# Optimization experiments

Measured on AMD Instinct MI355X. Metric: run time of the kernel, lower is better.

The kernel has to match this reference:

```python
import jax, jax.numpy as jnp
import numpy as np

N_NODES = 100000
N_EDGES = 400000
D = 128           # vector_dim
N_GRAPHS = 4096
N_LAYERS = 5
IN_FEAT = 11


def setup_inputs() -> dict:
    key = jax.random.key(0)
    ks = jax.random.split(key, 6)
    x = jax.random.uniform(ks[0], (N_NODES, IN_FEAT), dtype=jnp.float32)
    edge_index = jax.random.randint(ks[1], (2, N_EDGES), 0, N_NODES, dtype=jnp.int64)
    batch = jnp.sort(jax.random.randint(ks[2], (N_NODES,), 0, N_GRAPHS, dtype=jnp.int64))
    # expansion Linear(11, D)
    We = jax.random.normal(ks[3], (IN_FEAT, D), dtype=jnp.float32) * (1.0 / np.sqrt(IN_FEAT))
    be = jnp.zeros((D,), dtype=jnp.float32)
    # stacked GCNConv weights/biases for 5 layers
    Wg = jax.random.normal(ks[4], (N_LAYERS, D, D), dtype=jnp.float32) * (1.0 / np.sqrt(D))
    bg = jnp.zeros((N_LAYERS, D), dtype=jnp.float32)
    return {"x": x, "edge_index": edge_index, "batch": batch, "num_graphs": N_GRAPHS,
            "We": We, "be": be, "Wg": Wg, "bg": bg}


def reference(x, edge_index, batch, num_graphs, We, be, Wg, bg):
    n = x.shape[0]
    src, dst = edge_index[0], edge_index[1]
    # GCNConv(improved=True): self-loop weight 2 -> deg[i] = in_degree + 2
    deg = jax.ops.segment_sum(jnp.ones((src.shape[0],), x.dtype), dst, num_segments=n) + 2.0
    dinv = deg ** -0.5
    enorm = dinv[src] * dinv[dst]          # per-edge symmetric norm [E]
    self_norm = 2.0 * dinv * dinv          # self-loop contribution [N]

    h = jnp.log(x + 1.0) @ We + be         # expansion [N, D]
    for l in range(Wg.shape[0]):
        t = h @ Wg[l]                      # [N, D]
        agg = jax.ops.segment_sum(t[src] * enorm[:, None], dst, num_segments=n)
        agg = agg + self_norm[:, None] * t + bg[l]
        h = h + jax.nn.relu(agg)           # residual; dropout = identity (eval)
    return jax.ops.segment_sum(h, batch, num_segments=num_graphs)  # global_add_pool [G, D]
```

## Files before the change

### kernel.cpp

```cpp
#include <hip/hip_runtime.h>
#include <hip/hip_bf16.h>

#define NN 100000
#define NE 400000
#define DD 128
#define NG 4096
#define NL 5
#define NF 11
#define GROWS 100096

typedef __attribute__((ext_vector_type(8))) __bf16 bf16x8;
typedef __attribute__((ext_vector_type(4))) float f32x4;


__global__ void deg_kernel(const int* __restrict__ ei, int* __restrict__ deg) {
    int e = blockIdx.x * 256 + threadIdx.x;
    if (e < NE) atomicAdd(&deg[ei[NE + e]], 1);
}

__global__ void scan1_kernel(const int* __restrict__ deg, int* __restrict__ off,
                             int* __restrict__ bsums) {
    __shared__ int lds[256];
    int tid = threadIdx.x, b = blockIdx.x;
    int base = b * 1024 + tid * 4;
    int v[4];
#pragma unroll
    for (int q = 0; q < 4; ++q) {
        int i = base + q;
        v[q] = (i < NN) ? deg[i] : 0;
    }
    int s = v[0] + v[1] + v[2] + v[3];
    lds[tid] = s;
    __syncthreads();
    for (int o = 1; o < 256; o <<= 1) {
        int t2 = (tid >= o) ? lds[tid - o] : 0;
        __syncthreads();
        lds[tid] += t2;
        __syncthreads();
    }
    int p = lds[tid] - s;
#pragma unroll
    for (int q = 0; q < 4; ++q) {
        int i = base + q;
        if (i < NN) off[i] = p;
        p += v[q];
    }
    if (tid == 255) bsums[b] = lds[255];
}

__global__ void scan2_kernel(int* __restrict__ bsums, int nb) {
    __shared__ int lds[128];
    int tid = threadIdx.x;
    int v = (tid < nb) ? bsums[tid] : 0;
    lds[tid] = v;
    __syncthreads();
    for (int o = 1; o < 128; o <<= 1) {
        int t2 = (tid >= o) ? lds[tid - o] : 0;
        __syncthreads();
        lds[tid] += t2;
        __syncthreads();
    }
    if (tid < nb) bsums[tid] = lds[tid] - v;
}

__global__ void finish_kernel(int* __restrict__ off, const int* __restrict__ bsums,
                              const int* __restrict__ deg, float* __restrict__ dinv) {
    int i = blockIdx.x * 256 + threadIdx.x;
    if (i == 0) off[NN] = NE;
    if (i < NN) {
        off[i] += bsums[i >> 10];
        dinv[i] = rsqrtf((float)deg[i] + 2.0f);
    }
}

__global__ void fill_kernel(const int* __restrict__ ei, const int* __restrict__ off,
                            int* __restrict__ cursor, int2* __restrict__ csr,
                            const float* __restrict__ dinv) {
    int e = blockIdx.x * 256 + threadIdx.x;
    if (e >= NE) return;
    int s = ei[e];
    int d = ei[NE + e];
    int pos = off[d] + atomicAdd(&cursor[d], 1);
    csr[pos] = make_int2(s, __float_as_int(dinv[s] * dinv[d]));
}


__global__ void wpack_kernel(const float* __restrict__ Wg, unsigned short* __restrict__ whi,
                             unsigned short* __restrict__ wlo) {
    int t = blockIdx.x * 256 + threadIdx.x;
    int l = t >> 14, r = t & 16383;
    int k = r >> 7, n = r & 127;
    float w = Wg[(size_t)l * 16384 + k * 128 + n];
    __bf16 hb = (__bf16)w;
    float lo = w - (float)hb;
    __bf16 lb = (__bf16)lo;
    int ft = n >> 4, kc = k >> 5, lane = (((k >> 3) & 3) << 4) | (n & 15), i = k & 7;
    size_t idx = (size_t)l * 16384 + (((ft * 4 + kc) * 64 + lane) * 8 + i);
    whi[idx] = __builtin_bit_cast(unsigned short, hb);
    wlo[idx] = __builtin_bit_cast(unsigned short, lb);
}


__global__ __launch_bounds__(256) void expand_kernel(const float* __restrict__ x,
                                                     const float* __restrict__ We,
                                                     const float* __restrict__ be,
                                                     float* __restrict__ h) {
    __shared__ float ls[2 * NF];
    const int tid = threadIdx.x;
    const int node0 = blockIdx.x * 2;
    if (tid < 2 * NF) ls[tid] = __logf(x[(size_t)node0 * NF + tid] + 1.0f);
    __syncthreads();
    const int row = tid >> 7, j = tid & 127;
    float acc = be[j];
#pragma unroll
    for (int f = 0; f < NF; ++f) {
        acc = fmaf(ls[row * NF + f], We[f * DD + j], acc);
    }
    h[(size_t)(node0 + row) * DD + j] = acc;
}


__global__ __launch_bounds__(256) void agg_kernel(const float* __restrict__ h,
                                                  unsigned short* __restrict__ gbh,
                                                  unsigned short* __restrict__ gbl,
                                                  const int* __restrict__ off,
                                                  const int2* __restrict__ csr,
                                                  const float* __restrict__ dinv) {
    const int tid = threadIdx.x;
    const int node = blockIdx.x * 8 + (tid >> 5);
    const int jj = tid & 31;
    const float4* __restrict__ h4 = (const float4*)h;

    float di = dinv[node];
    float sn = 2.0f * di * di;
    float4 hv = h4[(size_t)node * 32 + jj];
    float4 acc = make_float4(sn * hv.x, sn * hv.y, sn * hv.z, sn * hv.w);

    const int e0 = off[node];
    const int e1 = off[node + 1];
#pragma unroll 1
    for (int e = e0; e < e1; e += 4) {
        const int eL = e1 - 1;
        int2 r0 = csr[e];
        int2 r1 = csr[min(e + 1, eL)];
        int2 r2 = csr[min(e + 2, eL)];
        int2 r3 = csr[min(e + 3, eL)];
        float4 v0 = h4[(size_t)r0.x * 32 + jj];
        float4 v1 = h4[(size_t)r1.x * 32 + jj];
        float4 v2 = h4[(size_t)r2.x * 32 + jj];
        float4 v3 = h4[(size_t)r3.x * 32 + jj];
        float w0 = __int_as_float(r0.y);
        float w1 = (e + 1 < e1) ? __int_as_float(r1.y) : 0.f;
        float w2 = (e + 2 < e1) ? __int_as_float(r2.y) : 0.f;
        float w3 = (e + 3 < e1) ? __int_as_float(r3.y) : 0.f;
        acc.x = fmaf(w0, v0.x, acc.x); acc.y = fmaf(w0, v0.y, acc.y);
        acc.z = fmaf(w0, v0.z, acc.z); acc.w = fmaf(w0, v0.w, acc.w);
        acc.x = fmaf(w1, v1.x, acc.x); acc.y = fmaf(w1, v1.y, acc.y);
        acc.z = fmaf(w1, v1.z, acc.z); acc.w = fmaf(w1, v1.w, acc.w);
        acc.x = fmaf(w2, v2.x, acc.x); acc.y = fmaf(w2, v2.y, acc.y);
        acc.z = fmaf(w2, v2.z, acc.z); acc.w = fmaf(w2, v2.w, acc.w);
        acc.x = fmaf(w3, v3.x, acc.x); acc.y = fmaf(w3, v3.y, acc.y);
        acc.z = fmaf(w3, v3.z, acc.z); acc.w = fmaf(w3, v3.w, acc.w);
    }

    __bf16 h0 = (__bf16)acc.x; __bf16 l0 = (__bf16)(acc.x - (float)h0);
    __bf16 h1 = (__bf16)acc.y; __bf16 l1 = (__bf16)(acc.y - (float)h1);
    __bf16 h2 = (__bf16)acc.z; __bf16 l2 = (__bf16)(acc.z - (float)h2);
    __bf16 h3 = (__bf16)acc.w; __bf16 l3 = (__bf16)(acc.w - (float)h3);
    const int tile = node >> 4;
    const int kc = jj >> 3;
    const int kg = (jj >> 1) & 3;
    const int i0 = (jj & 1) * 4;
    const int lanep = (kg << 4) | (node & 15);
    size_t base = (((size_t)tile * 4 + kc) * 64 + lanep) * 8 + i0;
    ushort4 hs = make_ushort4(__builtin_bit_cast(unsigned short, h0),
                              __builtin_bit_cast(unsigned short, h1),
                              __builtin_bit_cast(unsigned short, h2),
                              __builtin_bit_cast(unsigned short, h3));
    ushort4 ls = make_ushort4(__builtin_bit_cast(unsigned short, l0),
                              __builtin_bit_cast(unsigned short, l1),
                              __builtin_bit_cast(unsigned short, l2),
                              __builtin_bit_cast(unsigned short, l3));
    *(ushort4*)(gbh + base) = hs;
    *(ushort4*)(gbl + base) = ls;
}


__global__ __launch_bounds__(256) void mfma_gemm(const unsigned short* __restrict__ gbh,
                                                 const unsigned short* __restrict__ gbl,
                                                 float* __restrict__ h,
                                                 const unsigned short* __restrict__ whi,
                                                 const unsigned short* __restrict__ wlo,
                                                 const float* __restrict__ b) {
    const int lane = threadIdx.x & 63;
    const int wv = threadIdx.x >> 6;
    const int nbase = blockIdx.x * 64 + wv * 16;
    const size_t tbase = ((size_t)(nbase >> 4) * 4 * 64 + lane) * 8;

    bf16x8 gh[4], gl[4];
#pragma unroll
    for (int kc = 0; kc < 4; ++kc) {
        gh[kc] = *(const bf16x8*)(gbh + tbase + kc * 512);
        gl[kc] = *(const bf16x8*)(gbl + tbase + kc * 512);
    }

    f32x4 c[8];
#pragma unroll
    for (int ft = 0; ft < 8; ++ft) c[ft] = (f32x4){0.f, 0.f, 0.f, 0.f};

#pragma unroll
    for (int kc = 0; kc < 4; ++kc) {
#pragma unroll
        for (int ft = 0; ft < 8; ++ft) {
            size_t boff = (size_t)(((ft * 4 + kc) * 64 + lane) * 8);
            bf16x8 wh = *(const bf16x8*)(whi + boff);
            bf16x8 wl = *(const bf16x8*)(wlo + boff);
            c[ft] = __builtin_amdgcn_mfma_f32_16x16x32_bf16(wh, gh[kc], c[ft], 0, 0, 0);
            c[ft] = __builtin_amdgcn_mfma_f32_16x16x32_bf16(wl, gh[kc], c[ft], 0, 0, 0);
            c[ft] = __builtin_amdgcn_mfma_f32_16x16x32_bf16(wh, gl[kc], c[ft], 0, 0, 0);
        }
    }

    const int node = nbase + (lane & 15);
    const int f0 = (lane >> 4) * 4;
    if (node < NN) {
#pragma unroll
        for (int ft = 0; ft < 8; ++ft) {
            size_t o = (size_t)node * DD + ft * 16 + f0;
            float4 hv = *(const float4*)(h + o);
            float4 bv = *(const float4*)(b + ft * 16 + f0);
            hv.x += fmaxf(c[ft][0] + bv.x, 0.f);
            hv.y += fmaxf(c[ft][1] + bv.y, 0.f);
            hv.z += fmaxf(c[ft][2] + bv.z, 0.f);
            hv.w += fmaxf(c[ft][3] + bv.w, 0.f);
            *(float4*)(h + o) = hv;
        }
    }
}


__global__ void pool_kernel(const float* __restrict__ h, const int* __restrict__ batch,
                            float* __restrict__ out) {
    int j = threadIdx.x;
    int n0 = blockIdx.x * 64;
    float acc = 0.f;
    int prev = -1;
    for (int n = 0; n < 64; ++n) {
        int i = n0 + n;
        if (i >= NN) break;
        int bi = batch[i];
        if (bi != prev) {
            if (prev >= 0) atomicAdd(&out[(size_t)prev * DD + j], acc);
            acc = 0.f;
            prev = bi;
        }
        acc += h[(size_t)i * DD + j];
    }
    if (prev >= 0) atomicAdd(&out[(size_t)prev * DD + j], acc);
}


static inline size_t align_up(size_t x, size_t a) { return (x + a - 1) & ~(a - 1); }

extern "C" void kernel_launch(void* const* d_in, const int* in_sizes, int n_in,
                              void* d_out, int out_size, void* d_ws, size_t ws_size,
                              hipStream_t stream) {
    const float* x   = (const float*)d_in[0];
    const int*   ei  = (const int*)d_in[1];
    const int*   bat = (const int*)d_in[2];
    const float* We  = (const float*)d_in[4];
    const float* be  = (const float*)d_in[5];
    const float* Wg  = (const float*)d_in[6];
    const float* bg  = (const float*)d_in[7];
    float* out = (float*)d_out;

    char* p = (char*)d_ws;
    size_t o = 0;
    float* h = (float*)(p + o);       o = align_up(o + (size_t)NN * DD * 4, 512);
    unsigned short* gbh = (unsigned short*)(p + o); o = align_up(o + (size_t)GROWS * DD * 2, 512);
    unsigned short* gbl = (unsigned short*)(p + o); o = align_up(o + (size_t)GROWS * DD * 2, 512);
    float* dinv = (float*)(p + o);    o = align_up(o + (size_t)NN * 4, 512);
    int* deg = (int*)(p + o);         o = align_up(o + (size_t)NN * 4, 512);
    int* cursor = (int*)(p + o);      o = align_up(o + (size_t)NN * 4, 512);
    int* off = (int*)(p + o);         o = align_up(o + (size_t)(NN + 1) * 4, 512);
    int* bsums = (int*)(p + o);       o = align_up(o + 512, 512);
    int2* csr = (int2*)(p + o);       o = align_up(o + (size_t)NE * 8, 512);
    unsigned short* whi = (unsigned short*)(p + o); o = align_up(o + (size_t)NL * 16384 * 2, 512);
    unsigned short* wlo = (unsigned short*)(p + o); o = align_up(o + (size_t)NL * 16384 * 2, 512);
    (void)ws_size; (void)in_sizes; (void)n_in; (void)out_size;

    const int GRID_E = (NE + 255) / 256;
    const int GRID_SCAN1 = (NN + 1023) / 1024;
    const int GRID_N256 = (NN + 255) / 256;
    const int GRID_EXP = NN / 2;
    const int GRID_AGG = NN / 8;
    const int GRID_GEMM = GROWS / 64;
    const int GRID_POOL = (NN + 63) / 64;
    const int GRID_WPACK = NL * 16384 / 256;

    hipMemsetAsync(deg, 0, (size_t)NN * 4, stream);
    hipMemsetAsync(cursor, 0, (size_t)NN * 4, stream);
    hipMemsetAsync(out, 0, (size_t)NG * DD * 4, stream);

    deg_kernel<<<GRID_E, 256, 0, stream>>>(ei, deg);
    scan1_kernel<<<GRID_SCAN1, 256, 0, stream>>>(deg, off, bsums);
    scan2_kernel<<<1, 128, 0, stream>>>(bsums, GRID_SCAN1);
    finish_kernel<<<GRID_N256, 256, 0, stream>>>(off, bsums, deg, dinv);
    fill_kernel<<<GRID_E, 256, 0, stream>>>(ei, off, cursor, csr, dinv);
    wpack_kernel<<<GRID_WPACK, 256, 0, stream>>>(Wg, whi, wlo);

    expand_kernel<<<GRID_EXP, 256, 0, stream>>>(x, We, be, h);

    for (int l = 0; l < NL; ++l) {
        agg_kernel<<<GRID_AGG, 256, 0, stream>>>(h, gbh, gbl, off, csr, dinv);
        mfma_gemm<<<GRID_GEMM, 256, 0, stream>>>(gbh, gbl, h,
                                                 whi + (size_t)l * 16384,
                                                 wlo + (size_t)l * 16384,
                                                 bg + (size_t)l * DD);
    }

    pool_kernel<<<GRID_POOL, 128, 0, stream>>>(h, bat, out);
}
```

Baseline: 601.9 us.

## Interleave two nodes per group in aggregation and drop CSR cursor array

The aggregation kernel now has each 32-lane group process two adjacent nodes, issuing eight independent gathers per iteration so more memory requests are in flight. The CSR fill uses atomicAdd directly on the offset array, which turns it into end offsets and removes the separate cursor buffer and its memset. Edges past a node's range are masked to zero weight, but the loop runs until both nodes finish, so some loads are wasted when the two degrees differ.

```diff
diff --git a/kernel.cpp b/kernel.cpp
--- a/kernel.cpp
+++ b/kernel.cpp
@@ -66,21 +66,19 @@
 __global__ void finish_kernel(int* __restrict__ off, const int* __restrict__ bsums,
                               const int* __restrict__ deg, float* __restrict__ dinv) {
     int i = blockIdx.x * 256 + threadIdx.x;
-    if (i == 0) off[NN] = NE;
     if (i < NN) {
         off[i] += bsums[i >> 10];
         dinv[i] = rsqrtf((float)deg[i] + 2.0f);
     }
 }
 
-__global__ void fill_kernel(const int* __restrict__ ei, const int* __restrict__ off,
-                            int* __restrict__ cursor, int2* __restrict__ csr,
-                            const float* __restrict__ dinv) {
+__global__ void fill_kernel(const int* __restrict__ ei, int* __restrict__ off,
+                            int2* __restrict__ csr, const float* __restrict__ dinv) {
     int e = blockIdx.x * 256 + threadIdx.x;
     if (e >= NE) return;
     int s = ei[e];
     int d = ei[NE + e];
-    int pos = off[d] + atomicAdd(&cursor[d], 1);
+    int pos = atomicAdd(&off[d], 1);
     csr[pos] = make_int2(s, __float_as_int(dinv[s] * dinv[d]));
 }
 
@@ -120,49 +118,9 @@
 }
 
 
-__global__ __launch_bounds__(256) void agg_kernel(const float* __restrict__ h,
-                                                  unsigned short* __restrict__ gbh,
-                                                  unsigned short* __restrict__ gbl,
-                                                  const int* __restrict__ off,
-                                                  const int2* __restrict__ csr,
-                                                  const float* __restrict__ dinv) {
-    const int tid = threadIdx.x;
-    const int node = blockIdx.x * 8 + (tid >> 5);
-    const int jj = tid & 31;
-    const float4* __restrict__ h4 = (const float4*)h;
-
-    float di = dinv[node];
-    float sn = 2.0f * di * di;
-    float4 hv = h4[(size_t)node * 32 + jj];
-    float4 acc = make_float4(sn * hv.x, sn * hv.y, sn * hv.z, sn * hv.w);
-
-    const int e0 = off[node];
-    const int e1 = off[node + 1];
-#pragma unroll 1
-    for (int e = e0; e < e1; e += 4) {
-        const int eL = e1 - 1;
-        int2 r0 = csr[e];
-        int2 r1 = csr[min(e + 1, eL)];
-        int2 r2 = csr[min(e + 2, eL)];
-        int2 r3 = csr[min(e + 3, eL)];
-        float4 v0 = h4[(size_t)r0.x * 32 + jj];
-        float4 v1 = h4[(size_t)r1.x * 32 + jj];
-        float4 v2 = h4[(size_t)r2.x * 32 + jj];
-        float4 v3 = h4[(size_t)r3.x * 32 + jj];
-        float w0 = __int_as_float(r0.y);
-        float w1 = (e + 1 < e1) ? __int_as_float(r1.y) : 0.f;
-        float w2 = (e + 2 < e1) ? __int_as_float(r2.y) : 0.f;
-        float w3 = (e + 3 < e1) ? __int_as_float(r3.y) : 0.f;
-        acc.x = fmaf(w0, v0.x, acc.x); acc.y = fmaf(w0, v0.y, acc.y);
-        acc.z = fmaf(w0, v0.z, acc.z); acc.w = fmaf(w0, v0.w, acc.w);
-        acc.x = fmaf(w1, v1.x, acc.x); acc.y = fmaf(w1, v1.y, acc.y);
-        acc.z = fmaf(w1, v1.z, acc.z); acc.w = fmaf(w1, v1.w, acc.w);
-        acc.x = fmaf(w2, v2.x, acc.x); acc.y = fmaf(w2, v2.y, acc.y);
-        acc.z = fmaf(w2, v2.z, acc.z); acc.w = fmaf(w2, v2.w, acc.w);
-        acc.x = fmaf(w3, v3.x, acc.x); acc.y = fmaf(w3, v3.y, acc.y);
-        acc.z = fmaf(w3, v3.z, acc.z); acc.w = fmaf(w3, v3.w, acc.w);
-    }
-
+__device__ __forceinline__ void frag_store(unsigned short* __restrict__ gbh,
+                                           unsigned short* __restrict__ gbl,
+                                           int node, int jj, float4 acc) {
     __bf16 h0 = (__bf16)acc.x; __bf16 l0 = (__bf16)(acc.x - (float)h0);
     __bf16 h1 = (__bf16)acc.y; __bf16 l1 = (__bf16)(acc.y - (float)h1);
     __bf16 h2 = (__bf16)acc.z; __bf16 l2 = (__bf16)(acc.z - (float)h2);
@@ -173,16 +131,89 @@
     const int i0 = (jj & 1) * 4;
     const int lanep = (kg << 4) | (node & 15);
     size_t base = (((size_t)tile * 4 + kc) * 64 + lanep) * 8 + i0;
-    ushort4 hs = make_ushort4(__builtin_bit_cast(unsigned short, h0),
-                              __builtin_bit_cast(unsigned short, h1),
-                              __builtin_bit_cast(unsigned short, h2),
-                              __builtin_bit_cast(unsigned short, h3));
-    ushort4 ls = make_ushort4(__builtin_bit_cast(unsigned short, l0),
-                              __builtin_bit_cast(unsigned short, l1),
-                              __builtin_bit_cast(unsigned short, l2),
-                              __builtin_bit_cast(unsigned short, l3));
-    *(ushort4*)(gbh + base) = hs;
-    *(ushort4*)(gbl + base) = ls;
+    *(ushort4*)(gbh + base) = make_ushort4(__builtin_bit_cast(unsigned short, h0),
+                                           __builtin_bit_cast(unsigned short, h1),
+                                           __builtin_bit_cast(unsigned short, h2),
+                                           __builtin_bit_cast(unsigned short, h3));
+    *(ushort4*)(gbl + base) = make_ushort4(__builtin_bit_cast(unsigned short, l0),
+                                           __builtin_bit_cast(unsigned short, l1),
+                                           __builtin_bit_cast(unsigned short, l2),
+                                           __builtin_bit_cast(unsigned short, l3));
+}
+
+__global__ __launch_bounds__(256) void agg_kernel(const float* __restrict__ h,
+                                                  unsigned short* __restrict__ gbh,
+                                                  unsigned short* __restrict__ gbl,
+                                                  const int* __restrict__ off,
+                                                  const int2* __restrict__ csr,
+                                                  const float* __restrict__ dinv) {
+    const int tid = threadIdx.x;
+    const int grp = tid >> 5;
+    const int jj = tid & 31;
+    const int nodeA = blockIdx.x * 16 + grp * 2;
+    const int nodeB = nodeA + 1;
+    const float4* __restrict__ h4 = (const float4*)h;
+
+    float diA = dinv[nodeA], diB = dinv[nodeB];
+    float4 hvA = h4[(size_t)nodeA * 32 + jj];
+    float4 hvB = h4[(size_t)nodeB * 32 + jj];
+    float snA = 2.0f * diA * diA, snB = 2.0f * diB * diB;
+    float4 aA = make_float4(snA * hvA.x, snA * hvA.y, snA * hvA.z, snA * hvA.w);
+    float4 aB = make_float4(snB * hvB.x, snB * hvB.y, snB * hvB.z, snB * hvB.w);
+
+    const int e0A = (nodeA == 0) ? 0 : off[nodeA - 1];
+    const int e1A = off[nodeA];
+    const int e1B = off[nodeB];
+    int eA = e0A, eB = e1A;
+
+#pragma unroll 1
+    while (eA < e1A || eB < e1B) {
+        int2 rA0 = csr[min(eA,     NE - 1)];
+        int2 rA1 = csr[min(eA + 1, NE - 1)];
+        int2 rA2 = csr[min(eA + 2, NE - 1)];
+        int2 rA3 = csr[min(eA + 3, NE - 1)];
+        int2 rB0 = csr[min(eB,     NE - 1)];
+        int2 rB1 = csr[min(eB + 1, NE - 1)];
+        int2 rB2 = csr[min(eB + 2, NE - 1)];
+        int2 rB3 = csr[min(eB + 3, NE - 1)];
+        float4 vA0 = h4[(size_t)rA0.x * 32 + jj];
+        float4 vA1 = h4[(size_t)rA1.x * 32 + jj];
+        float4 vA2 = h4[(size_t)rA2.x * 32 + jj];
+        float4 vA3 = h4[(size_t)rA3.x * 32 + jj];
+        float4 vB0 = h4[(size_t)rB0.x * 32 + jj];
+        float4 vB1 = h4[(size_t)rB1.x * 32 + jj];
+        float4 vB2 = h4[(size_t)rB2.x * 32 + jj];
+        float4 vB3 = h4[(size_t)rB3.x * 32 + jj];
+        float wA0 = (eA     < e1A) ? __int_as_float(rA0.y) : 0.f;
+        float wA1 = (eA + 1 < e1A) ? __int_as_float(rA1.y) : 0.f;
+        float wA2 = (eA + 2 < e1A) ? __int_as_float(rA2.y) : 0.f;
+        float wA3 = (eA + 3 < e1A) ? __int_as_float(rA3.y) : 0.f;
+        float wB0 = (eB     < e1B) ? __int_as_float(rB0.y) : 0.f;
+        float wB1 = (eB + 1 < e1B) ? __int_as_float(rB1.y) : 0.f;
+        float wB2 = (eB + 2 < e1B) ? __int_as_float(rB2.y) : 0.f;
+        float wB3 = (eB + 3 < e1B) ? __int_as_float(rB3.y) : 0.f;
+        aA.x = fmaf(wA0, vA0.x, aA.x); aA.y = fmaf(wA0, vA0.y, aA.y);
+        aA.z = fmaf(wA0, vA0.z, aA.z); aA.w = fmaf(wA0, vA0.w, aA.w);
+        aA.x = fmaf(wA1, vA1.x, aA.x); aA.y = fmaf(wA1, vA1.y, aA.y);
+        aA.z = fmaf(wA1, vA1.z, aA.z); aA.w = fmaf(wA1, vA1.w, aA.w);
+        aA.x = fmaf(wA2, vA2.x, aA.x); aA.y = fmaf(wA2, vA2.y, aA.y);
+        aA.z = fmaf(wA2, vA2.z, aA.z); aA.w = fmaf(wA2, vA2.w, aA.w);
+        aA.x = fmaf(wA3, vA3.x, aA.x); aA.y = fmaf(wA3, vA3.y, aA.y);
+        aA.z = fmaf(wA3, vA3.z, aA.z); aA.w = fmaf(wA3, vA3.w, aA.w);
+        aB.x = fmaf(wB0, vB0.x, aB.x); aB.y = fmaf(wB0, vB0.y, aB.y);
+        aB.z = fmaf(wB0, vB0.z, aB.z); aB.w = fmaf(wB0, vB0.w, aB.w);
+        aB.x = fmaf(wB1, vB1.x, aB.x); aB.y = fmaf(wB1, vB1.y, aB.y);
+        aB.z = fmaf(wB1, vB1.z, aB.z); aB.w = fmaf(wB1, vB1.w, aB.w);
+        aB.x = fmaf(wB2, vB2.x, aB.x); aB.y = fmaf(wB2, vB2.y, aB.y);
+        aB.z = fmaf(wB2, vB2.z, aB.z); aB.w = fmaf(wB2, vB2.w, aB.w);
+        aB.x = fmaf(wB3, vB3.x, aB.x); aB.y = fmaf(wB3, vB3.y, aB.y);
+        aB.z = fmaf(wB3, vB3.z, aB.z); aB.w = fmaf(wB3, vB3.w, aB.w);
+        eA += 4;
+        eB += 4;
+    }
+
+    frag_store(gbh, gbl, nodeA, jj, aA);
+    frag_store(gbh, gbl, nodeB, jj, aB);
 }
 
 
@@ -281,7 +312,6 @@
     unsigned short* gbl = (unsigned short*)(p + o); o = align_up(o + (size_t)GROWS * DD * 2, 512);
     float* dinv = (float*)(p + o);    o = align_up(o + (size_t)NN * 4, 512);
     int* deg = (int*)(p + o);         o = align_up(o + (size_t)NN * 4, 512);
-    int* cursor = (int*)(p + o);      o = align_up(o + (size_t)NN * 4, 512);
     int* off = (int*)(p + o);         o = align_up(o + (size_t)(NN + 1) * 4, 512);
     int* bsums = (int*)(p + o);       o = align_up(o + 512, 512);
     int2* csr = (int2*)(p + o);       o = align_up(o + (size_t)NE * 8, 512);
@@ -293,20 +323,19 @@
     const int GRID_SCAN1 = (NN + 1023) / 1024;
     const int GRID_N256 = (NN + 255) / 256;
     const int GRID_EXP = NN / 2;
-    const int GRID_AGG = NN / 8;
+    const int GRID_AGG = NN / 16;
     const int GRID_GEMM = GROWS / 64;
     const int GRID_POOL = (NN + 63) / 64;
     const int GRID_WPACK = NL * 16384 / 256;
 
     hipMemsetAsync(deg, 0, (size_t)NN * 4, stream);
-    hipMemsetAsync(cursor, 0, (size_t)NN * 4, stream);
     hipMemsetAsync(out, 0, (size_t)NG * DD * 4, stream);
 
     deg_kernel<<<GRID_E, 256, 0, stream>>>(ei, deg);
     scan1_kernel<<<GRID_SCAN1, 256, 0, stream>>>(deg, off, bsums);
     scan2_kernel<<<1, 128, 0, stream>>>(bsums, GRID_SCAN1);
     finish_kernel<<<GRID_N256, 256, 0, stream>>>(off, bsums, deg, dinv);
-    fill_kernel<<<GRID_E, 256, 0, stream>>>(ei, off, cursor, csr, dinv);
+    fill_kernel<<<GRID_E, 256, 0, stream>>>(ei, off, csr, dinv);
     wpack_kernel<<<GRID_WPACK, 256, 0, stream>>>(Wg, whi, wlo);
 
     expand_kernel<<<GRID_EXP, 256, 0, stream>>>(x, We, be, h);
```

Result: slower. 624.8 us (+3.8%).
